# Kernel optimization log

Measured on AMD Instinct MI355X. Metric: run time of the kernel, lower is better.

Reference implementation:

```python
import jax, jax.numpy as jnp
import numpy as np

N_NODES = 100000
N_EDGES = 1000000
H = 128


def setup_inputs() -> dict:
    key = jax.random.key(0)
    ks = jax.random.split(key, 8)
    s = 1.0 / np.sqrt(H)
    return {
        "x": jax.random.normal(ks[0], (N_NODES, H), dtype=jnp.float32),
        "edge_index": jax.random.randint(ks[1], (2, N_EDGES), 0, N_NODES, dtype=jnp.int64),
        "W_p": jax.random.normal(ks[2], (H, H), dtype=jnp.float32) * s,
        "b_p": jnp.zeros((H,), dtype=jnp.float32),
        "W_c": jax.random.normal(ks[3], (H, H), dtype=jnp.float32) * s,
        "b_c": jnp.zeros((H,), dtype=jnp.float32),
        "W1": jax.random.normal(ks[4], (3 * H, H), dtype=jnp.float32) * (1.0 / np.sqrt(3 * H)),
        "b1": jnp.zeros((H,), dtype=jnp.float32),
        "W2": jax.random.normal(ks[5], (H, 1), dtype=jnp.float32) * s,
        "b2": jnp.zeros((1,), dtype=jnp.float32),
    }


def reference(x, edge_index, W_p, b_p, W_c, b_c, W1, b1, W2, b2):
    # Gather parent (src) and child (dst) node features per edge: [E, H]
    par_fea = x[edge_index[0]]
    cld_fea = x[edge_index[1]]
    # Dual small MLPs (LeakyReLU slope 0.01, dropout inactive at inference)
    enc_p = jax.nn.leaky_relu(par_fea @ W_p + b_p, negative_slope=0.01)
    enc_c = jax.nn.leaky_relu(cld_fea @ W_c + b_c, negative_slope=0.01)
    diff = jnp.abs(par_fea - cld_fea)
    edge_features = jnp.concatenate([enc_p, enc_c, diff], axis=-1)  # [E, 3H]
    h = jax.nn.relu(edge_features @ W1 + b1)
    edge_weight = jax.nn.sigmoid(h @ W2 + b2).squeeze(-1)  # [E]
    return edge_weight
```

## Files before the change

### kernel.cpp

```cpp
#include <hip/hip_runtime.h>
#include <hip/hip_bf16.h>

#define E_EDGES 1000000
#define N_NODES 100000
#define HDIM 128
#define BM 64
#define LDP 136
#define REC 384

typedef __attribute__((ext_vector_type(8))) short short8;
typedef __attribute__((ext_vector_type(4))) float f32x4;

static __device__ __forceinline__ short f2bf(float f) {
  unsigned int u = __float_as_uint(f);
  unsigned int r = (u + 0x7FFFu + ((u >> 16) & 1u)) >> 16;
  return (short)r;
}
static __device__ __forceinline__ float bf2f(short s) {
  return __uint_as_float(((unsigned int)(unsigned short)s) << 16);
}
static __device__ __forceinline__ unsigned int bfsub_abs2(unsigned int a, unsigned int b) {
  __hip_bfloat162 x, y;
  __builtin_memcpy(&x, &a, 4);
  __builtin_memcpy(&y, &b, 4);
  __hip_bfloat162 r = __habs2(__hsub2(x, y));
  unsigned int u;
  __builtin_memcpy(&u, &r, 4);
  return u;
}
static __device__ __forceinline__ unsigned int bfadd2(unsigned int a, unsigned int b) {
  __hip_bfloat162 x, y;
  __builtin_memcpy(&x, &a, 4);
  __builtin_memcpy(&y, &b, 4);
  __hip_bfloat162 r = __hadd2(x, y);
  unsigned int u;
  __builtin_memcpy(&u, &r, 4);
  return u;
}

__global__ void prep_weights(const float* __restrict__ Wp, const float* __restrict__ Wc,
                             const float* __restrict__ W1, const float* __restrict__ W2,
                             short* __restrict__ wp_t, short* __restrict__ wc_t,
                             short* __restrict__ w1_t, float* __restrict__ w2v) {
  int i = blockIdx.x * 256 + threadIdx.x;
  if (i < HDIM * HDIM) {
    int o = i >> 7, k = i & (HDIM - 1);
    wp_t[i] = f2bf(Wp[k * HDIM + o]);
    wc_t[i] = f2bf(Wc[k * HDIM + o]);
  }
  if (i < HDIM * 3 * HDIM) {
    int o = i / (3 * HDIM), k = i - o * (3 * HDIM);
    w1_t[i] = f2bf(W1[k * HDIM + o]);
  }
  if (i < HDIM) w2v[i] = W2[i];
}

__global__ __launch_bounds__(256) void node_precompute(
    const float* __restrict__ x, const float* __restrict__ b_p,
    const float* __restrict__ b_c, const float* __restrict__ b1,
    const short* __restrict__ wp_t, const short* __restrict__ wc_t,
    const short* __restrict__ w1_t, short* __restrict__ rec) {
  __shared__ __align__(16) short Xt[BM * LDP];
  __shared__ __align__(16) short Yp[BM * LDP];
  __shared__ __align__(16) short Yc[BM * LDP];

  const int t = threadIdx.x;
  const int n0 = blockIdx.x * BM;

  {
    const int lane16 = t & 15, rq = t >> 4, c0 = lane16 * 8;
#pragma unroll
    for (int pass = 0; pass < 4; ++pass) {
      const int row = pass * 16 + rq;
      const int n = n0 + row;
      short8 v;
      if (n < N_NODES) {
        const float* ps = x + (size_t)n * HDIM + c0;
        float4 a = *(const float4*)ps;
        float4 b = *(const float4*)(ps + 4);
        float f[8] = {a.x, a.y, a.z, a.w, b.x, b.y, b.z, b.w};
#pragma unroll
        for (int j = 0; j < 8; ++j) v[j] = f2bf(f[j]);
        *(short8*)&rec[(size_t)n * REC + c0] = v;
      } else {
#pragma unroll
        for (int j = 0; j < 8; ++j) v[j] = 0;
      }
      *(short8*)&Xt[row * LDP + c0] = v;
    }
  }
  __syncthreads();

  const int l = t & 63;
  const int w = t >> 6;
  const int lr = l & 15;
  const int lg = l >> 4;
  const int aoff = lr * LDP + lg * 8;
  const int na = w * 32 + lr, nb = na + 16;

  const f32x4 zero4 = {0.f, 0.f, 0.f, 0.f};
  f32x4 ap_[4][2], ac_[4][2];
#pragma unroll
  for (int mi = 0; mi < 4; ++mi) {
    ap_[mi][0] = zero4; ap_[mi][1] = zero4;
    ac_[mi][0] = zero4; ac_[mi][1] = zero4;
  }

  const short* wpA = wp_t + na * HDIM + lg * 8;
  const short* wpB = wp_t + nb * HDIM + lg * 8;
  const short* wcA = wc_t + na * HDIM + lg * 8;
  const short* wcB = wc_t + nb * HDIM + lg * 8;

#pragma unroll
  for (int kk = 0; kk < 4; ++kk) {
    short8 b10 = *(const short8*)(wpA + kk * 32);
    short8 b11 = *(const short8*)(wpB + kk * 32);
    short8 b20 = *(const short8*)(wcA + kk * 32);
    short8 b21 = *(const short8*)(wcB + kk * 32);
#pragma unroll
    for (int mi = 0; mi < 4; ++mi) {
      short8 a8 = *(const short8*)&Xt[mi * 16 * LDP + aoff + kk * 32];
      ap_[mi][0] = __builtin_amdgcn_mfma_f32_16x16x32_bf16(a8, b10, ap_[mi][0], 0, 0, 0);
      ap_[mi][1] = __builtin_amdgcn_mfma_f32_16x16x32_bf16(a8, b11, ap_[mi][1], 0, 0, 0);
      ac_[mi][0] = __builtin_amdgcn_mfma_f32_16x16x32_bf16(a8, b20, ac_[mi][0], 0, 0, 0);
      ac_[mi][1] = __builtin_amdgcn_mfma_f32_16x16x32_bf16(a8, b21, ac_[mi][1], 0, 0, 0);
    }
  }

  {
    const float bpa = b_p[na], bpb = b_p[nb];
    const float bca = b_c[na], bcb = b_c[nb];
#pragma unroll
    for (int mi = 0; mi < 4; ++mi) {
#pragma unroll
      for (int r = 0; r < 4; ++r) {
        const int m = mi * 16 + lg * 4 + r;
        float v0 = ap_[mi][0][r] + bpa; v0 = v0 > 0.f ? v0 : 0.01f * v0;
        float v1 = ap_[mi][1][r] + bpb; v1 = v1 > 0.f ? v1 : 0.01f * v1;
        float u0 = ac_[mi][0][r] + bca; u0 = u0 > 0.f ? u0 : 0.01f * u0;
        float u1 = ac_[mi][1][r] + bcb; u1 = u1 > 0.f ? u1 : 0.01f * u1;
        Yp[m * LDP + na] = f2bf(v0);
        Yp[m * LDP + nb] = f2bf(v1);
        Yc[m * LDP + na] = f2bf(u0);
        Yc[m * LDP + nb] = f2bf(u1);
      }
    }
  }
  __syncthreads();

  f32x4 aa_[4][2], ab_[4][2];
#pragma unroll
  for (int mi = 0; mi < 4; ++mi) {
    aa_[mi][0] = zero4; aa_[mi][1] = zero4;
    ab_[mi][0] = zero4; ab_[mi][1] = zero4;
  }
  const short* w1Aa = w1_t + na * (3 * HDIM) + lg * 8;
  const short* w1Ab = w1_t + nb * (3 * HDIM) + lg * 8;
#pragma unroll
  for (int kk = 0; kk < 4; ++kk) {
    short8 ba0 = *(const short8*)(w1Aa + kk * 32);
    short8 ba1 = *(const short8*)(w1Ab + kk * 32);
    short8 bb0 = *(const short8*)(w1Aa + HDIM + kk * 32);
    short8 bb1 = *(const short8*)(w1Ab + HDIM + kk * 32);
#pragma unroll
    for (int mi = 0; mi < 4; ++mi) {
      short8 ayp = *(const short8*)&Yp[mi * 16 * LDP + aoff + kk * 32];
      short8 ayc = *(const short8*)&Yc[mi * 16 * LDP + aoff + kk * 32];
      aa_[mi][0] = __builtin_amdgcn_mfma_f32_16x16x32_bf16(ayp, ba0, aa_[mi][0], 0, 0, 0);
      aa_[mi][1] = __builtin_amdgcn_mfma_f32_16x16x32_bf16(ayp, ba1, aa_[mi][1], 0, 0, 0);
      ab_[mi][0] = __builtin_amdgcn_mfma_f32_16x16x32_bf16(ayc, bb0, ab_[mi][0], 0, 0, 0);
      ab_[mi][1] = __builtin_amdgcn_mfma_f32_16x16x32_bf16(ayc, bb1, ab_[mi][1], 0, 0, 0);
    }
  }

  {
    const float b1a = b1[na], b1b = b1[nb];
#pragma unroll
    for (int mi = 0; mi < 4; ++mi) {
#pragma unroll
      for (int r = 0; r < 4; ++r) {
        const int m = mi * 16 + lg * 4 + r;
        const int n = n0 + m;
        if (n < N_NODES) {
          short* rn = rec + (size_t)n * REC;
          rn[HDIM + na] = f2bf(aa_[mi][0][r] + b1a);
          rn[HDIM + nb] = f2bf(aa_[mi][1][r] + b1b);
          rn[2 * HDIM + na] = f2bf(ab_[mi][0][r]);
          rn[2 * HDIM + nb] = f2bf(ab_[mi][1][r]);
        }
      }
    }
  }
}

__global__ __launch_bounds__(512, 8) void edge_kernel(
    const int* __restrict__ ei, const short* __restrict__ rec,
    const short* __restrict__ w1_t, const float* __restrict__ w2v,
    const float* __restrict__ b2, float* __restrict__ out) {
  __shared__ __align__(16) short Dt[BM * LDP];
  __shared__ __align__(16) short St[BM * LDP];
  __shared__ float partial[8][BM];

  const int t = threadIdx.x;
  const int e0 = blockIdx.x * BM;

  {
    const int lane16 = t & 15, rq = t >> 4, c0 = lane16 * 8;
#pragma unroll
    for (int pass = 0; pass < 2; ++pass) {
      const int row = pass * 32 + rq;
      const int s = ei[e0 + row];
      const int d = ei[E_EDGES + e0 + row];
      const short* rs = rec + (size_t)s * REC + c0;
      const short* rd = rec + (size_t)d * REC + c0;
      uint4 p = *(const uint4*)rs;
      uint4 a = *(const uint4*)(rs + HDIM);
      uint4 c = *(const uint4*)rd;
      uint4 b = *(const uint4*)(rd + 2 * HDIM);
      uint4 vd, vs;
      vd.x = bfsub_abs2(p.x, c.x);
      vd.y = bfsub_abs2(p.y, c.y);
      vd.z = bfsub_abs2(p.z, c.z);
      vd.w = bfsub_abs2(p.w, c.w);
      vs.x = bfadd2(a.x, b.x);
      vs.y = bfadd2(a.y, b.y);
      vs.z = bfadd2(a.z, b.z);
      vs.w = bfadd2(a.w, b.w);
      *(uint4*)&Dt[row * LDP + c0] = vd;
      *(uint4*)&St[row * LDP + c0] = vs;
    }
  }
  __syncthreads();

  const int l = t & 63;
  const int w = t >> 6;
  const int lr = l & 15;
  const int lg = l >> 4;
  const int aoff = lr * LDP + lg * 8;

  f32x4 acc[4];
  const int scol = w * 16 + lg * 4;
#pragma unroll
  for (int mi = 0; mi < 4; ++mi) {
    uint2 u = *(const uint2*)&St[(mi * 16 + lr) * LDP + scol];
    acc[mi][0] = __uint_as_float(u.x << 16);
    acc[mi][1] = __uint_as_float(u.x & 0xffff0000u);
    acc[mi][2] = __uint_as_float(u.y << 16);
    acc[mi][3] = __uint_as_float(u.y & 0xffff0000u);
  }

  const int na = w * 16 + lr;
  const short* w1D = w1_t + na * (3 * HDIM) + 2 * HDIM + lg * 8;
#pragma unroll
  for (int kk = 0; kk < 4; ++kk) {
    short8 b8 = *(const short8*)(w1D + kk * 32);
#pragma unroll
    for (int mi = 0; mi < 4; ++mi) {
      short8 a8 = *(const short8*)&Dt[mi * 16 * LDP + aoff + kk * 32];
      acc[mi] = __builtin_amdgcn_mfma_f32_16x16x32_bf16(b8, a8, acc[mi], 0, 0, 0);
    }
  }

  {
    const float4 w2q = *(const float4*)&w2v[w * 16 + lg * 4];
#pragma unroll
    for (int mi = 0; mi < 4; ++mi) {
      float p = fmaxf(acc[mi][0], 0.f) * w2q.x + fmaxf(acc[mi][1], 0.f) * w2q.y +
                fmaxf(acc[mi][2], 0.f) * w2q.z + fmaxf(acc[mi][3], 0.f) * w2q.w;
      p += __shfl_xor(p, 16);
      p += __shfl_xor(p, 32);
      if (lg == 0) partial[w][mi * 16 + lr] = p;
    }
  }
  __syncthreads();

  if (t < BM) {
    float z = partial[0][t] + partial[1][t] + partial[2][t] + partial[3][t] +
              partial[4][t] + partial[5][t] + partial[6][t] + partial[7][t] + b2[0];
    out[e0 + t] = 1.0f / (1.0f + __expf(-z));
  }
}

__global__ __launch_bounds__(512, 4) void edge_weight_fallback(
    const float* __restrict__ x, const int* __restrict__ ei,
    const float* __restrict__ b_p, const float* __restrict__ b_c,
    const float* __restrict__ b1, const float* __restrict__ b2,
    const short* __restrict__ wp_t, const short* __restrict__ wc_t,
    const short* __restrict__ w1_t, const float* __restrict__ w2v,
    float* __restrict__ out) {
  __shared__ __align__(16) short Pt[BM * LDP];
  __shared__ __align__(16) short Ct[BM * LDP];
  __shared__ __align__(16) short Dt[BM * LDP];
  __shared__ float partial[8][BM];

  const int t = threadIdx.x;
  const int e0 = blockIdx.x * BM;
  {
    const int lane16 = t & 15, rq = t >> 4, c0 = lane16 * 8;
#pragma unroll
    for (int pass = 0; pass < 2; ++pass) {
      const int row = pass * 32 + rq;
      const int ip = ei[e0 + row];
      const int ic = ei[E_EDGES + e0 + row];
      const float* ps = x + (size_t)ip * HDIM + c0;
      const float* cs = x + (size_t)ic * HDIM + c0;
      float4 pa = *(const float4*)ps, pb = *(const float4*)(ps + 4);
      float4 ca = *(const float4*)cs, cb = *(const float4*)(cs + 4);
      float pf[8] = {pa.x, pa.y, pa.z, pa.w, pb.x, pb.y, pb.z, pb.w};
      float cf[8] = {ca.x, ca.y, ca.z, ca.w, cb.x, cb.y, cb.z, cb.w};
      short8 vp, vc, vd;
#pragma unroll
      for (int j = 0; j < 8; ++j) {
        vp[j] = f2bf(pf[j]); vc[j] = f2bf(cf[j]); vd[j] = f2bf(fabsf(pf[j] - cf[j]));
      }
      *(short8*)&Pt[row * LDP + c0] = vp;
      *(short8*)&Ct[row * LDP + c0] = vc;
      *(short8*)&Dt[row * LDP + c0] = vd;
    }
  }
  __syncthreads();
  const int l = t & 63, w = t >> 6, lr = l & 15, lg = l >> 4;
  const int n0 = w * 16, na = n0 + lr, aoff = lr * LDP + lg * 8;
  const f32x4 zero4 = {0.f, 0.f, 0.f, 0.f};
  f32x4 acc1[4], acc2[4], acc3[4];
#pragma unroll
  for (int mi = 0; mi < 4; ++mi) { acc1[mi] = zero4; acc2[mi] = zero4; acc3[mi] = zero4; }
  const short* wpA = wp_t + na * HDIM + lg * 8;
  const short* wcA = wc_t + na * HDIM + lg * 8;
  const short* w1A = w1_t + na * (3 * HDIM) + lg * 8;
#pragma unroll
  for (int kk = 0; kk < 4; ++kk) {
    short8 bp8 = *(const short8*)(wpA + kk * 32);
    short8 bc8 = *(const short8*)(wcA + kk * 32);
    short8 bd8 = *(const short8*)(w1A + 2 * HDIM + kk * 32);
#pragma unroll
    for (int mi = 0; mi < 4; ++mi) {
      short8 ap = *(const short8*)&Pt[mi * 16 * LDP + aoff + kk * 32];
      short8 ac = *(const short8*)&Ct[mi * 16 * LDP + aoff + kk * 32];
      short8 ad = *(const short8*)&Dt[mi * 16 * LDP + aoff + kk * 32];
      acc1[mi] = __builtin_amdgcn_mfma_f32_16x16x32_bf16(ap, bp8, acc1[mi], 0, 0, 0);
      acc2[mi] = __builtin_amdgcn_mfma_f32_16x16x32_bf16(ac, bc8, acc2[mi], 0, 0, 0);
      acc3[mi] = __builtin_amdgcn_mfma_f32_16x16x32_bf16(ad, bd8, acc3[mi], 0, 0, 0);
    }
  }
  __syncthreads();
  {
    const float bpa = b_p[na], bca = b_c[na];
#pragma unroll
    for (int mi = 0; mi < 4; ++mi) {
#pragma unroll
      for (int r = 0; r < 4; ++r) {
        const int m = mi * 16 + lg * 4 + r;
        float v0 = acc1[mi][r] + bpa; v0 = v0 > 0.f ? v0 : 0.01f * v0;
        float u0 = acc2[mi][r] + bca; u0 = u0 > 0.f ? u0 : 0.01f * u0;
        Pt[m * LDP + na] = f2bf(v0);
        Ct[m * LDP + na] = f2bf(u0);
      }
    }
  }
  __syncthreads();
#pragma unroll
  for (int kk = 0; kk < 4; ++kk) {
    short8 b0 = *(const short8*)(w1A + kk * 32);
    short8 b1f = *(const short8*)(w1A + HDIM + kk * 32);
#pragma unroll
    for (int mi = 0; mi < 4; ++mi) {
      short8 a0 = *(const short8*)&Pt[mi * 16 * LDP + aoff + kk * 32];
      short8 a1 = *(const short8*)&Ct[mi * 16 * LDP + aoff + kk * 32];
      acc3[mi] = __builtin_amdgcn_mfma_f32_16x16x32_bf16(a0, b0, acc3[mi], 0, 0, 0);
      acc3[mi] = __builtin_amdgcn_mfma_f32_16x16x32_bf16(a1, b1f, acc3[mi], 0, 0, 0);
    }
  }
  {
    const float b1a = b1[na], w2a = w2v[na];
#pragma unroll
    for (int mi = 0; mi < 4; ++mi) {
#pragma unroll
      for (int r = 0; r < 4; ++r) {
        float h0 = acc3[mi][r] + b1a; h0 = h0 > 0.f ? h0 : 0.f;
        float v = h0 * w2a;
        v += __shfl_xor(v, 1); v += __shfl_xor(v, 2);
        v += __shfl_xor(v, 4); v += __shfl_xor(v, 8);
        if (lr == 0) partial[w][mi * 16 + lg * 4 + r] = v;
      }
    }
  }
  __syncthreads();
  if (t < BM) {
    float z = partial[0][t] + partial[1][t] + partial[2][t] + partial[3][t] +
              partial[4][t] + partial[5][t] + partial[6][t] + partial[7][t] + b2[0];
    out[e0 + t] = 1.0f / (1.0f + __expf(-z));
  }
}

extern "C" void kernel_launch(void* const* d_in, const int* in_sizes, int n_in,
                              void* d_out, int out_size, void* d_ws, size_t ws_size,
                              hipStream_t stream) {
  const float* x  = (const float*)d_in[0];
  const int*   ei = (const int*)d_in[1];
  const float* Wp = (const float*)d_in[2];
  const float* bp = (const float*)d_in[3];
  const float* Wc = (const float*)d_in[4];
  const float* bc = (const float*)d_in[5];
  const float* W1 = (const float*)d_in[6];
  const float* b1 = (const float*)d_in[7];
  const float* W2 = (const float*)d_in[8];
  const float* b2 = (const float*)d_in[9];
  float* out = (float*)d_out;

  short* wp_t = (short*)d_ws;
  short* wc_t = wp_t + HDIM * HDIM;
  short* w1_t = wc_t + HDIM * HDIM;
  float* w2v  = (float*)(w1_t + HDIM * 3 * HDIM);
  short* rec  = (short*)(w2v + HDIM);

  const size_t needed = (size_t)((char*)(rec + (size_t)N_NODES * REC) - (char*)d_ws);
  const int nblocks = E_EDGES / BM;

  prep_weights<<<(HDIM * 3 * HDIM + 255) / 256, 256, 0, stream>>>(Wp, Wc, W1, W2,
                                                                  wp_t, wc_t, w1_t, w2v);
  if (ws_size >= needed) {
    node_precompute<<<(N_NODES + BM - 1) / BM, 256, 0, stream>>>(
        x, bp, bc, b1, wp_t, wc_t, w1_t, rec);
    edge_kernel<<<nblocks, 512, 0, stream>>>(ei, rec, w1_t, w2v, b2, out);
  } else {
    edge_weight_fallback<<<nblocks, 512, 0, stream>>>(x, ei, bp, bc, b1, b2,
                                                      wp_t, wc_t, w1_t, w2v, out);
  }
}
```

Baseline: 198.2 us.

## Process two edge tiles per block with prefetched gathers; coalesce node record stores

```diff
diff --git a/kernel.cpp b/kernel.cpp
--- a/kernel.cpp
+++ b/kernel.cpp
@@ -60,34 +60,31 @@
     const float* __restrict__ b_c, const float* __restrict__ b1,
     const short* __restrict__ wp_t, const short* __restrict__ wc_t,
     const short* __restrict__ w1_t, short* __restrict__ rec) {
-  __shared__ __align__(16) short Xt[BM * LDP];
-  __shared__ __align__(16) short Yp[BM * LDP];
-  __shared__ __align__(16) short Yc[BM * LDP];
+  __shared__ __align__(16) short Buf1[BM * LDP];
+  __shared__ __align__(16) short Buf2[BM * LDP];
 
   const int t = threadIdx.x;
   const int n0 = blockIdx.x * BM;
-
-  {
-    const int lane16 = t & 15, rq = t >> 4, c0 = lane16 * 8;
-#pragma unroll
-    for (int pass = 0; pass < 4; ++pass) {
-      const int row = pass * 16 + rq;
-      const int n = n0 + row;
-      short8 v;
-      if (n < N_NODES) {
-        const float* ps = x + (size_t)n * HDIM + c0;
-        float4 a = *(const float4*)ps;
-        float4 b = *(const float4*)(ps + 4);
-        float f[8] = {a.x, a.y, a.z, a.w, b.x, b.y, b.z, b.w};
-#pragma unroll
-        for (int j = 0; j < 8; ++j) v[j] = f2bf(f[j]);
-        *(short8*)&rec[(size_t)n * REC + c0] = v;
-      } else {
-#pragma unroll
-        for (int j = 0; j < 8; ++j) v[j] = 0;
-      }
-      *(short8*)&Xt[row * LDP + c0] = v;
-    }
+  const int lane16 = t & 15, rq = t >> 4, c0 = lane16 * 8;
+
+#pragma unroll
+  for (int pass = 0; pass < 4; ++pass) {
+    const int row = pass * 16 + rq;
+    const int n = n0 + row;
+    short8 v;
+    if (n < N_NODES) {
+      const float* ps = x + (size_t)n * HDIM + c0;
+      float4 a = *(const float4*)ps;
+      float4 b = *(const float4*)(ps + 4);
+      float f[8] = {a.x, a.y, a.z, a.w, b.x, b.y, b.z, b.w};
+#pragma unroll
+      for (int j = 0; j < 8; ++j) v[j] = f2bf(f[j]);
+      *(short8*)&rec[(size_t)n * REC + c0] = v;
+    } else {
+#pragma unroll
+      for (int j = 0; j < 8; ++j) v[j] = 0;
+    }
+    *(short8*)&Buf1[row * LDP + c0] = v;
   }
   __syncthreads();
 
@@ -119,13 +116,14 @@
     short8 b21 = *(const short8*)(wcB + kk * 32);
 #pragma unroll
     for (int mi = 0; mi < 4; ++mi) {
-      short8 a8 = *(const short8*)&Xt[mi * 16 * LDP + aoff + kk * 32];
+      short8 a8 = *(const short8*)&Buf1[mi * 16 * LDP + aoff + kk * 32];
       ap_[mi][0] = __builtin_amdgcn_mfma_f32_16x16x32_bf16(a8, b10, ap_[mi][0], 0, 0, 0);
       ap_[mi][1] = __builtin_amdgcn_mfma_f32_16x16x32_bf16(a8, b11, ap_[mi][1], 0, 0, 0);
       ac_[mi][0] = __builtin_amdgcn_mfma_f32_16x16x32_bf16(a8, b20, ac_[mi][0], 0, 0, 0);
       ac_[mi][1] = __builtin_amdgcn_mfma_f32_16x16x32_bf16(a8, b21, ac_[mi][1], 0, 0, 0);
     }
   }
+  __syncthreads();
 
   {
     const float bpa = b_p[na], bpb = b_p[nb];
@@ -139,10 +137,10 @@
         float v1 = ap_[mi][1][r] + bpb; v1 = v1 > 0.f ? v1 : 0.01f * v1;
         float u0 = ac_[mi][0][r] + bca; u0 = u0 > 0.f ? u0 : 0.01f * u0;
         float u1 = ac_[mi][1][r] + bcb; u1 = u1 > 0.f ? u1 : 0.01f * u1;
-        Yp[m * LDP + na] = f2bf(v0);
-        Yp[m * LDP + nb] = f2bf(v1);
-        Yc[m * LDP + na] = f2bf(u0);
-        Yc[m * LDP + nb] = f2bf(u1);
+        Buf2[m * LDP + na] = f2bf(v0);
+        Buf2[m * LDP + nb] = f2bf(v1);
+        Buf1[m * LDP + na] = f2bf(u0);
+        Buf1[m * LDP + nb] = f2bf(u1);
       }
     }
   }
@@ -164,14 +162,15 @@
     short8 bb1 = *(const short8*)(w1Ab + HDIM + kk * 32);
 #pragma unroll
     for (int mi = 0; mi < 4; ++mi) {
-      short8 ayp = *(const short8*)&Yp[mi * 16 * LDP + aoff + kk * 32];
-      short8 ayc = *(const short8*)&Yc[mi * 16 * LDP + aoff + kk * 32];
+      short8 ayp = *(const short8*)&Buf2[mi * 16 * LDP + aoff + kk * 32];
+      short8 ayc = *(const short8*)&Buf1[mi * 16 * LDP + aoff + kk * 32];
       aa_[mi][0] = __builtin_amdgcn_mfma_f32_16x16x32_bf16(ayp, ba0, aa_[mi][0], 0, 0, 0);
       aa_[mi][1] = __builtin_amdgcn_mfma_f32_16x16x32_bf16(ayp, ba1, aa_[mi][1], 0, 0, 0);
       ab_[mi][0] = __builtin_amdgcn_mfma_f32_16x16x32_bf16(ayc, bb0, ab_[mi][0], 0, 0, 0);
       ab_[mi][1] = __builtin_amdgcn_mfma_f32_16x16x32_bf16(ayc, bb1, ab_[mi][1], 0, 0, 0);
     }
   }
+  __syncthreads();
 
   {
     const float b1a = b1[na], b1b = b1[nb];
@@ -180,20 +179,28 @@
 #pragma unroll
       for (int r = 0; r < 4; ++r) {
         const int m = mi * 16 + lg * 4 + r;
-        const int n = n0 + m;
-        if (n < N_NODES) {
-          short* rn = rec + (size_t)n * REC;
-          rn[HDIM + na] = f2bf(aa_[mi][0][r] + b1a);
-          rn[HDIM + nb] = f2bf(aa_[mi][1][r] + b1b);
-          rn[2 * HDIM + na] = f2bf(ab_[mi][0][r]);
-          rn[2 * HDIM + nb] = f2bf(ab_[mi][1][r]);
-        }
-      }
-    }
-  }
-}
-
-__global__ __launch_bounds__(512, 8) void edge_kernel(
+        Buf2[m * LDP + na] = f2bf(aa_[mi][0][r] + b1a);
+        Buf2[m * LDP + nb] = f2bf(aa_[mi][1][r] + b1b);
+        Buf1[m * LDP + na] = f2bf(ab_[mi][0][r]);
+        Buf1[m * LDP + nb] = f2bf(ab_[mi][1][r]);
+      }
+    }
+  }
+  __syncthreads();
+
+#pragma unroll
+  for (int pass = 0; pass < 4; ++pass) {
+    const int row = pass * 16 + rq;
+    const int n = n0 + row;
+    if (n < N_NODES) {
+      short* rn = rec + (size_t)n * REC;
+      *(short8*)&rn[HDIM + c0] = *(const short8*)&Buf2[row * LDP + c0];
+      *(short8*)&rn[2 * HDIM + c0] = *(const short8*)&Buf1[row * LDP + c0];
+    }
+  }
+}
+
+__global__ __launch_bounds__(512, 6) void edge_kernel(
     const int* __restrict__ ei, const short* __restrict__ rec,
     const short* __restrict__ w1_t, const float* __restrict__ w2v,
     const float* __restrict__ b2, float* __restrict__ out) {
@@ -202,67 +209,86 @@
   __shared__ float partial[8][BM];
 
   const int t = threadIdx.x;
-  const int e0 = blockIdx.x * BM;
-
-  {
-    const int lane16 = t & 15, rq = t >> 4, c0 = lane16 * 8;
-#pragma unroll
-    for (int pass = 0; pass < 2; ++pass) {
-      const int row = pass * 32 + rq;
-      const int s = ei[e0 + row];
-      const int d = ei[E_EDGES + e0 + row];
-      const short* rs = rec + (size_t)s * REC + c0;
-      const short* rd = rec + (size_t)d * REC + c0;
-      uint4 p = *(const uint4*)rs;
-      uint4 a = *(const uint4*)(rs + HDIM);
-      uint4 c = *(const uint4*)rd;
-      uint4 b = *(const uint4*)(rd + 2 * HDIM);
-      uint4 vd, vs;
-      vd.x = bfsub_abs2(p.x, c.x);
-      vd.y = bfsub_abs2(p.y, c.y);
-      vd.z = bfsub_abs2(p.z, c.z);
-      vd.w = bfsub_abs2(p.w, c.w);
-      vs.x = bfadd2(a.x, b.x);
-      vs.y = bfadd2(a.y, b.y);
-      vs.z = bfadd2(a.z, b.z);
-      vs.w = bfadd2(a.w, b.w);
-      *(uint4*)&Dt[row * LDP + c0] = vd;
-      *(uint4*)&St[row * LDP + c0] = vs;
-    }
-  }
-  __syncthreads();
+  const int lane16 = t & 15, rq = t >> 4, c0 = lane16 * 8;
+  const int e0A = blockIdx.x * 2 * BM;
+  const int e0B = e0A + BM;
+  const bool hasB = (e0B < E_EDGES);
 
   const int l = t & 63;
   const int w = t >> 6;
   const int lr = l & 15;
   const int lg = l >> 4;
   const int aoff = lr * LDP + lg * 8;
-
-  f32x4 acc[4];
+  const int na = w * 16 + lr;
   const int scol = w * 16 + lg * 4;
-#pragma unroll
-  for (int mi = 0; mi < 4; ++mi) {
-    uint2 u = *(const uint2*)&St[(mi * 16 + lr) * LDP + scol];
-    acc[mi][0] = __uint_as_float(u.x << 16);
-    acc[mi][1] = __uint_as_float(u.x & 0xffff0000u);
-    acc[mi][2] = __uint_as_float(u.y << 16);
-    acc[mi][3] = __uint_as_float(u.y & 0xffff0000u);
-  }
-
-  const int na = w * 16 + lr;
   const short* w1D = w1_t + na * (3 * HDIM) + 2 * HDIM + lg * 8;
-#pragma unroll
-  for (int kk = 0; kk < 4; ++kk) {
-    short8 b8 = *(const short8*)(w1D + kk * 32);
-#pragma unroll
-    for (int mi = 0; mi < 4; ++mi) {
-      short8 a8 = *(const short8*)&Dt[mi * 16 * LDP + aoff + kk * 32];
-      acc[mi] = __builtin_amdgcn_mfma_f32_16x16x32_bf16(b8, a8, acc[mi], 0, 0, 0);
-    }
-  }
-
-  {
-    const float4 w2q = *(const float4*)&w2v[w * 16 + lg * 4];
+  const float4 w2q = *(const float4*)&w2v[w * 16 + lg * 4];
+
+  const int rowLo = rq, rowHi = 32 + rq;
+  int sA0 = ei[e0A + rowLo], dA0 = ei[E_EDGES + e0A + rowLo];
+  int sA1 = ei[e0A + rowHi], dA1 = ei[E_EDGES + e0A + rowHi];
+  int sB0 = 0, dB0 = 0, sB1 = 0, dB1 = 0;
+  if (hasB) {
+    sB0 = ei[e0B + rowLo]; dB0 = ei[E_EDGES + e0B + rowLo];
+    sB1 = ei[e0B + rowHi]; dB1 = ei[E_EDGES + e0B + rowHi];
+  }
+  const short* rsA0 = rec + (size_t)sA0 * REC + c0;
+  const short* rdA0 = rec + (size_t)dA0 * REC + c0;
+  const short* rsA1 = rec + (size_t)sA1 * REC + c0;
+  const short* rdA1 = rec + (size_t)dA1 * REC + c0;
+  uint4 pA0 = *(const uint4*)rsA0, aA0 = *(const uint4*)(rsA0 + HDIM);
+  uint4 cA0 = *(const uint4*)rdA0, bA0 = *(const uint4*)(rdA0 + 2 * HDIM);
+  uint4 pA1 = *(const uint4*)rsA1, aA1 = *(const uint4*)(rsA1 + HDIM);
+  uint4 cA1 = *(const uint4*)rdA1, bA1 = *(const uint4*)(rdA1 + 2 * HDIM);
+
+  {
+    uint4 vd, vs;
+    vd.x = bfsub_abs2(pA0.x, cA0.x); vd.y = bfsub_abs2(pA0.y, cA0.y);
+    vd.z = bfsub_abs2(pA0.z, cA0.z); vd.w = bfsub_abs2(pA0.w, cA0.w);
+    vs.x = bfadd2(aA0.x, bA0.x); vs.y = bfadd2(aA0.y, bA0.y);
+    vs.z = bfadd2(aA0.z, bA0.z); vs.w = bfadd2(aA0.w, bA0.w);
+    *(uint4*)&Dt[rowLo * LDP + c0] = vd;
+    *(uint4*)&St[rowLo * LDP + c0] = vs;
+    vd.x = bfsub_abs2(pA1.x, cA1.x); vd.y = bfsub_abs2(pA1.y, cA1.y);
+    vd.z = bfsub_abs2(pA1.z, cA1.z); vd.w = bfsub_abs2(pA1.w, cA1.w);
+    vs.x = bfadd2(aA1.x, bA1.x); vs.y = bfadd2(aA1.y, bA1.y);
+    vs.z = bfadd2(aA1.z, bA1.z); vs.w = bfadd2(aA1.w, bA1.w);
+    *(uint4*)&Dt[rowHi * LDP + c0] = vd;
+    *(uint4*)&St[rowHi * LDP + c0] = vs;
+  }
+
+  uint4 pB0, aB0, cB0, bB0, pB1, aB1, cB1, bB1;
+  if (hasB) {
+    const short* rsB0 = rec + (size_t)sB0 * REC + c0;
+    const short* rdB0 = rec + (size_t)dB0 * REC + c0;
+    const short* rsB1 = rec + (size_t)sB1 * REC + c0;
+    const short* rdB1 = rec + (size_t)dB1 * REC + c0;
+    pB0 = *(const uint4*)rsB0; aB0 = *(const uint4*)(rsB0 + HDIM);
+    cB0 = *(const uint4*)rdB0; bB0 = *(const uint4*)(rdB0 + 2 * HDIM);
+    pB1 = *(const uint4*)rsB1; aB1 = *(const uint4*)(rsB1 + HDIM);
+    cB1 = *(const uint4*)rdB1; bB1 = *(const uint4*)(rdB1 + 2 * HDIM);
+  }
+  __syncthreads();
+
+  auto do_tile = [&](int ebase) {
+    f32x4 acc[4];
+#pragma unroll
+    for (int mi = 0; mi < 4; ++mi) {
+      uint2 u = *(const uint2*)&St[(mi * 16 + lr) * LDP + scol];
+      acc[mi][0] = __uint_as_float(u.x << 16);
+      acc[mi][1] = __uint_as_float(u.x & 0xffff0000u);
+      acc[mi][2] = __uint_as_float(u.y << 16);
+      acc[mi][3] = __uint_as_float(u.y & 0xffff0000u);
+    }
+#pragma unroll
+    for (int kk = 0; kk < 4; ++kk) {
+      short8 b8 = *(const short8*)(w1D + kk * 32);
+#pragma unroll
+      for (int mi = 0; mi < 4; ++mi) {
+        short8 a8 = *(const short8*)&Dt[mi * 16 * LDP + aoff + kk * 32];
+        acc[mi] = __builtin_amdgcn_mfma_f32_16x16x32_bf16(b8, a8, acc[mi], 0, 0, 0);
+      }
+    }
 #pragma unroll
     for (int mi = 0; mi < 4; ++mi) {
       float p = fmaxf(acc[mi][0], 0.f) * w2q.x + fmaxf(acc[mi][1], 0.f) * w2q.y +
@@ -271,13 +297,32 @@
       p += __shfl_xor(p, 32);
       if (lg == 0) partial[w][mi * 16 + lr] = p;
     }
-  }
-  __syncthreads();
-
-  if (t < BM) {
-    float z = partial[0][t] + partial[1][t] + partial[2][t] + partial[3][t] +
-              partial[4][t] + partial[5][t] + partial[6][t] + partial[7][t] + b2[0];
-    out[e0 + t] = 1.0f / (1.0f + __expf(-z));
+    __syncthreads();
+    if (t < BM) {
+      float z = partial[0][t] + partial[1][t] + partial[2][t] + partial[3][t] +
+                partial[4][t] + partial[5][t] + partial[6][t] + partial[7][t] + b2[0];
+      out[ebase + t] = 1.0f / (1.0f + __expf(-z));
+    }
+  };
+
+  do_tile(e0A);
+
+  if (hasB) {
+    uint4 vd, vs;
+    vd.x = bfsub_abs2(pB0.x, cB0.x); vd.y = bfsub_abs2(pB0.y, cB0.y);
+    vd.z = bfsub_abs2(pB0.z, cB0.z); vd.w = bfsub_abs2(pB0.w, cB0.w);
+    vs.x = bfadd2(aB0.x, bB0.x); vs.y = bfadd2(aB0.y, bB0.y);
+    vs.z = bfadd2(aB0.z, bB0.z); vs.w = bfadd2(aB0.w, bB0.w);
+    *(uint4*)&Dt[rowLo * LDP + c0] = vd;
+    *(uint4*)&St[rowLo * LDP + c0] = vs;
+    vd.x = bfsub_abs2(pB1.x, cB1.x); vd.y = bfsub_abs2(pB1.y, cB1.y);
+    vd.z = bfsub_abs2(pB1.z, cB1.z); vd.w = bfsub_abs2(pB1.w, cB1.w);
+    vs.x = bfadd2(aB1.x, bB1.x); vs.y = bfadd2(aB1.y, bB1.y);
+    vs.z = bfadd2(aB1.z, bB1.z); vs.w = bfadd2(aB1.w, bB1.w);
+    *(uint4*)&Dt[rowHi * LDP + c0] = vd;
+    *(uint4*)&St[rowHi * LDP + c0] = vs;
+    __syncthreads();
+    do_tile(e0B);
   }
 }
 
@@ -415,16 +460,16 @@
   short* rec  = (short*)(w2v + HDIM);
 
   const size_t needed = (size_t)((char*)(rec + (size_t)N_NODES * REC) - (char*)d_ws);
-  const int nblocks = E_EDGES / BM;
+  const int ntiles = E_EDGES / BM;
 
   prep_weights<<<(HDIM * 3 * HDIM + 255) / 256, 256, 0, stream>>>(Wp, Wc, W1, W2,
                                                                   wp_t, wc_t, w1_t, w2v);
   if (ws_size >= needed) {
     node_precompute<<<(N_NODES + BM - 1) / BM, 256, 0, stream>>>(
         x, bp, bc, b1, wp_t, wc_t, w1_t, rec);
-    edge_kernel<<<nblocks, 512, 0, stream>>>(ei, rec, w1_t, w2v, b2, out);
+    edge_kernel<<<(ntiles + 1) / 2, 512, 0, stream>>>(ei, rec, w1_t, w2v, b2, out);
   } else {
-    edge_weight_fallback<<<nblocks, 512, 0, stream>>>(x, ei, bp, bc, b1, b2,
-                                                      wp_t, wc_t, w1_t, w2v, out);
-  }
-}
+    edge_weight_fallback<<<ntiles, 512, 0, stream>>>(x, ei, bp, bc, b1, b2,
+                                                     wp_t, wc_t, w1_t, w2v, out);
+  }
+}
```

New measurement: 204.3 us. +3.1%, slower.

## Widen node_precompute to 512 threads, reuse LDS buffers, stage output stores

Applied to the files above, without the earlier changes.

```diff
diff --git a/kernel.cpp b/kernel.cpp
--- a/kernel.cpp
+++ b/kernel.cpp
@@ -55,39 +55,36 @@
   if (i < HDIM) w2v[i] = W2[i];
 }
 
-__global__ __launch_bounds__(256) void node_precompute(
+__global__ __launch_bounds__(512, 8) void node_precompute(
     const float* __restrict__ x, const float* __restrict__ b_p,
     const float* __restrict__ b_c, const float* __restrict__ b1,
     const short* __restrict__ wp_t, const short* __restrict__ wc_t,
     const short* __restrict__ w1_t, short* __restrict__ rec) {
-  __shared__ __align__(16) short Xt[BM * LDP];
-  __shared__ __align__(16) short Yp[BM * LDP];
-  __shared__ __align__(16) short Yc[BM * LDP];
+  __shared__ __align__(16) short Buf1[BM * LDP];
+  __shared__ __align__(16) short Buf2[BM * LDP];
 
   const int t = threadIdx.x;
   const int n0 = blockIdx.x * BM;
-
-  {
-    const int lane16 = t & 15, rq = t >> 4, c0 = lane16 * 8;
-#pragma unroll
-    for (int pass = 0; pass < 4; ++pass) {
-      const int row = pass * 16 + rq;
-      const int n = n0 + row;
-      short8 v;
-      if (n < N_NODES) {
-        const float* ps = x + (size_t)n * HDIM + c0;
-        float4 a = *(const float4*)ps;
-        float4 b = *(const float4*)(ps + 4);
-        float f[8] = {a.x, a.y, a.z, a.w, b.x, b.y, b.z, b.w};
-#pragma unroll
-        for (int j = 0; j < 8; ++j) v[j] = f2bf(f[j]);
-        *(short8*)&rec[(size_t)n * REC + c0] = v;
-      } else {
-#pragma unroll
-        for (int j = 0; j < 8; ++j) v[j] = 0;
-      }
-      *(short8*)&Xt[row * LDP + c0] = v;
-    }
+  const int lane16 = t & 15, rq = t >> 4, c0 = lane16 * 8;
+
+#pragma unroll
+  for (int pass = 0; pass < 2; ++pass) {
+    const int row = pass * 32 + rq;
+    const int n = n0 + row;
+    short8 v;
+    if (n < N_NODES) {
+      const float* ps = x + (size_t)n * HDIM + c0;
+      float4 a = *(const float4*)ps;
+      float4 b = *(const float4*)(ps + 4);
+      float f[8] = {a.x, a.y, a.z, a.w, b.x, b.y, b.z, b.w};
+#pragma unroll
+      for (int j = 0; j < 8; ++j) v[j] = f2bf(f[j]);
+      *(short8*)&rec[(size_t)n * REC + c0] = v;
+    } else {
+#pragma unroll
+      for (int j = 0; j < 8; ++j) v[j] = 0;
+    }
+    *(short8*)&Buf1[row * LDP + c0] = v;
   }
   __syncthreads();
 
@@ -96,99 +93,86 @@
   const int lr = l & 15;
   const int lg = l >> 4;
   const int aoff = lr * LDP + lg * 8;
-  const int na = w * 32 + lr, nb = na + 16;
+  const int na = w * 16 + lr;
 
   const f32x4 zero4 = {0.f, 0.f, 0.f, 0.f};
-  f32x4 ap_[4][2], ac_[4][2];
-#pragma unroll
-  for (int mi = 0; mi < 4; ++mi) {
-    ap_[mi][0] = zero4; ap_[mi][1] = zero4;
-    ac_[mi][0] = zero4; ac_[mi][1] = zero4;
-  }
+  f32x4 ap_[4], ac_[4];
+#pragma unroll
+  for (int mi = 0; mi < 4; ++mi) { ap_[mi] = zero4; ac_[mi] = zero4; }
 
   const short* wpA = wp_t + na * HDIM + lg * 8;
-  const short* wpB = wp_t + nb * HDIM + lg * 8;
   const short* wcA = wc_t + na * HDIM + lg * 8;
-  const short* wcB = wc_t + nb * HDIM + lg * 8;
 
 #pragma unroll
   for (int kk = 0; kk < 4; ++kk) {
-    short8 b10 = *(const short8*)(wpA + kk * 32);
-    short8 b11 = *(const short8*)(wpB + kk * 32);
-    short8 b20 = *(const short8*)(wcA + kk * 32);
-    short8 b21 = *(const short8*)(wcB + kk * 32);
-#pragma unroll
-    for (int mi = 0; mi < 4; ++mi) {
-      short8 a8 = *(const short8*)&Xt[mi * 16 * LDP + aoff + kk * 32];
-      ap_[mi][0] = __builtin_amdgcn_mfma_f32_16x16x32_bf16(a8, b10, ap_[mi][0], 0, 0, 0);
-      ap_[mi][1] = __builtin_amdgcn_mfma_f32_16x16x32_bf16(a8, b11, ap_[mi][1], 0, 0, 0);
-      ac_[mi][0] = __builtin_amdgcn_mfma_f32_16x16x32_bf16(a8, b20, ac_[mi][0], 0, 0, 0);
-      ac_[mi][1] = __builtin_amdgcn_mfma_f32_16x16x32_bf16(a8, b21, ac_[mi][1], 0, 0, 0);
-    }
-  }
-
-  {
-    const float bpa = b_p[na], bpb = b_p[nb];
-    const float bca = b_c[na], bcb = b_c[nb];
+    short8 bp8 = *(const short8*)(wpA + kk * 32);
+    short8 bc8 = *(const short8*)(wcA + kk * 32);
+#pragma unroll
+    for (int mi = 0; mi < 4; ++mi) {
+      short8 a8 = *(const short8*)&Buf1[mi * 16 * LDP + aoff + kk * 32];
+      ap_[mi] = __builtin_amdgcn_mfma_f32_16x16x32_bf16(a8, bp8, ap_[mi], 0, 0, 0);
+      ac_[mi] = __builtin_amdgcn_mfma_f32_16x16x32_bf16(a8, bc8, ac_[mi], 0, 0, 0);
+    }
+  }
+  __syncthreads();
+
+  {
+    const float bpa = b_p[na];
+    const float bca = b_c[na];
 #pragma unroll
     for (int mi = 0; mi < 4; ++mi) {
 #pragma unroll
       for (int r = 0; r < 4; ++r) {
         const int m = mi * 16 + lg * 4 + r;
-        float v0 = ap_[mi][0][r] + bpa; v0 = v0 > 0.f ? v0 : 0.01f * v0;
-        float v1 = ap_[mi][1][r] + bpb; v1 = v1 > 0.f ? v1 : 0.01f * v1;
-        float u0 = ac_[mi][0][r] + bca; u0 = u0 > 0.f ? u0 : 0.01f * u0;
-        float u1 = ac_[mi][1][r] + bcb; u1 = u1 > 0.f ? u1 : 0.01f * u1;
-        Yp[m * LDP + na] = f2bf(v0);
-        Yp[m * LDP + nb] = f2bf(v1);
-        Yc[m * LDP + na] = f2bf(u0);
-        Yc[m * LDP + nb] = f2bf(u1);
+        float v0 = ap_[mi][r] + bpa; v0 = v0 > 0.f ? v0 : 0.01f * v0;
+        float u0 = ac_[mi][r] + bca; u0 = u0 > 0.f ? u0 : 0.01f * u0;
+        Buf2[m * LDP + na] = f2bf(v0);
+        Buf1[m * LDP + na] = f2bf(u0);
       }
     }
   }
   __syncthreads();
 
-  f32x4 aa_[4][2], ab_[4][2];
-#pragma unroll
-  for (int mi = 0; mi < 4; ++mi) {
-    aa_[mi][0] = zero4; aa_[mi][1] = zero4;
-    ab_[mi][0] = zero4; ab_[mi][1] = zero4;
-  }
+  f32x4 aa_[4], ab_[4];
+#pragma unroll
+  for (int mi = 0; mi < 4; ++mi) { aa_[mi] = zero4; ab_[mi] = zero4; }
   const short* w1Aa = w1_t + na * (3 * HDIM) + lg * 8;
-  const short* w1Ab = w1_t + nb * (3 * HDIM) + lg * 8;
 #pragma unroll
   for (int kk = 0; kk < 4; ++kk) {
-    short8 ba0 = *(const short8*)(w1Aa + kk * 32);
-    short8 ba1 = *(const short8*)(w1Ab + kk * 32);
-    short8 bb0 = *(const short8*)(w1Aa + HDIM + kk * 32);
-    short8 bb1 = *(const short8*)(w1Ab + HDIM + kk * 32);
-#pragma unroll
-    for (int mi = 0; mi < 4; ++mi) {
-      short8 ayp = *(const short8*)&Yp[mi * 16 * LDP + aoff + kk * 32];
-      short8 ayc = *(const short8*)&Yc[mi * 16 * LDP + aoff + kk * 32];
-      aa_[mi][0] = __builtin_amdgcn_mfma_f32_16x16x32_bf16(ayp, ba0, aa_[mi][0], 0, 0, 0);
-      aa_[mi][1] = __builtin_amdgcn_mfma_f32_16x16x32_bf16(ayp, ba1, aa_[mi][1], 0, 0, 0);
-      ab_[mi][0] = __builtin_amdgcn_mfma_f32_16x16x32_bf16(ayc, bb0, ab_[mi][0], 0, 0, 0);
-      ab_[mi][1] = __builtin_amdgcn_mfma_f32_16x16x32_bf16(ayc, bb1, ab_[mi][1], 0, 0, 0);
-    }
-  }
-
-  {
-    const float b1a = b1[na], b1b = b1[nb];
+    short8 ba = *(const short8*)(w1Aa + kk * 32);
+    short8 bb = *(const short8*)(w1Aa + HDIM + kk * 32);
+#pragma unroll
+    for (int mi = 0; mi < 4; ++mi) {
+      short8 ayp = *(const short8*)&Buf2[mi * 16 * LDP + aoff + kk * 32];
+      short8 ayc = *(const short8*)&Buf1[mi * 16 * LDP + aoff + kk * 32];
+      aa_[mi] = __builtin_amdgcn_mfma_f32_16x16x32_bf16(ayp, ba, aa_[mi], 0, 0, 0);
+      ab_[mi] = __builtin_amdgcn_mfma_f32_16x16x32_bf16(ayc, bb, ab_[mi], 0, 0, 0);
+    }
+  }
+  __syncthreads();
+
+  {
+    const float b1a = b1[na];
 #pragma unroll
     for (int mi = 0; mi < 4; ++mi) {
 #pragma unroll
       for (int r = 0; r < 4; ++r) {
         const int m = mi * 16 + lg * 4 + r;
-        const int n = n0 + m;
-        if (n < N_NODES) {
-          short* rn = rec + (size_t)n * REC;
-          rn[HDIM + na] = f2bf(aa_[mi][0][r] + b1a);
-          rn[HDIM + nb] = f2bf(aa_[mi][1][r] + b1b);
-          rn[2 * HDIM + na] = f2bf(ab_[mi][0][r]);
-          rn[2 * HDIM + nb] = f2bf(ab_[mi][1][r]);
-        }
+        Buf2[m * LDP + na] = f2bf(aa_[mi][r] + b1a);
+        Buf1[m * LDP + na] = f2bf(ab_[mi][r]);
       }
+    }
+  }
+  __syncthreads();
+
+#pragma unroll
+  for (int pass = 0; pass < 2; ++pass) {
+    const int row = pass * 32 + rq;
+    const int n = n0 + row;
+    if (n < N_NODES) {
+      short* rn = rec + (size_t)n * REC;
+      *(short8*)&rn[HDIM + c0] = *(const short8*)&Buf2[row * LDP + c0];
+      *(short8*)&rn[2 * HDIM + c0] = *(const short8*)&Buf1[row * LDP + c0];
     }
   }
 }
@@ -415,16 +399,16 @@
   short* rec  = (short*)(w2v + HDIM);
 
   const size_t needed = (size_t)((char*)(rec + (size_t)N_NODES * REC) - (char*)d_ws);
-  const int nblocks = E_EDGES / BM;
+  const int ntiles = E_EDGES / BM;
 
   prep_weights<<<(HDIM * 3 * HDIM + 255) / 256, 256, 0, stream>>>(Wp, Wc, W1, W2,
                                                                   wp_t, wc_t, w1_t, w2v);
   if (ws_size >= needed) {
-    node_precompute<<<(N_NODES + BM - 1) / BM, 256, 0, stream>>>(
+    node_precompute<<<(N_NODES + BM - 1) / BM, 512, 0, stream>>>(
         x, bp, bc, b1, wp_t, wc_t, w1_t, rec);
-    edge_kernel<<<nblocks, 512, 0, stream>>>(ei, rec, w1_t, w2v, b2, out);
+    edge_kernel<<<ntiles, 512, 0, stream>>>(ei, rec, w1_t, w2v, b2, out);
   } else {
-    edge_weight_fallback<<<nblocks, 512, 0, stream>>>(x, ei, bp, bc, b1, b2,
-                                                      wp_t, wc_t, w1_t, w2v, out);
-  }
-}
+    edge_weight_fallback<<<ntiles, 512, 0, stream>>>(x, ei, bp, bc, b1, b2,
+                                                     wp_t, wc_t, w1_t, w2v, out);
+  }
+}
```

After: 193.6 us. 2.3% less time.
